# Performance work log

Hardware: AMD Instinct MI355X
Metric: run time of the kernel (lower is better)

Reference implementation:

```python
import jax, jax.numpy as jnp
import numpy as np

D_MODEL = 256
D_STATE = 64
D_CONV = 4
EXPAND = 2
HEADDIM = 64
D_INNER = EXPAND * D_MODEL          # 512
NHEADS = D_INNER // HEADDIM         # 8
CONV_DIM = D_INNER + 2 * D_STATE    # 640
D_IN_PROJ = 2 * D_INNER + 2 * D_STATE + NHEADS  # 1160
BATCH = 4
SEQ = 4096  # H*W = 64*64


def _silu(x):
    return x * jax.nn.sigmoid(x)


def _layernorm(x, w, b, eps=1e-5):
    mu = jnp.mean(x, axis=-1, keepdims=True)
    xc = x - mu
    var = jnp.mean(xc * xc, axis=-1, keepdims=True)
    return xc * jax.lax.rsqrt(var + eps) * w + b


def _mamba2(x, W_in, conv_w, conv_b, dt_bias, A_log, D_param, rms_w, W_out):
    # x: (B, L, d_model)
    B, L, _ = x.shape
    zxbcdt = x @ W_in.T                                   # (B,L,1160)
    z = zxbcdt[..., :D_INNER]                             # gate (B,L,512)
    xBC = zxbcdt[..., D_INNER:D_INNER + CONV_DIM]         # (B,L,640)
    dt = jax.nn.softplus(zxbcdt[..., -NHEADS:] + dt_bias) # (B,L,8)
    # causal depthwise conv (kernel D_CONV) + SiLU
    xp = jnp.pad(xBC, ((0, 0), (D_CONV - 1, 0), (0, 0)))
    xBC = sum(xp[:, k:k + L, :] * conv_w[:, k] for k in range(D_CONV)) + conv_b
    xBC = _silu(xBC)
    xh = xBC[..., :D_INNER].reshape(B, L, NHEADS, HEADDIM)
    Bm = xBC[..., D_INNER:D_INNER + D_STATE]              # (B,L,64), ngroups=1
    Cm = xBC[..., D_INNER + D_STATE:]                     # (B,L,64)
    dA = jnp.exp(dt * (-jnp.exp(A_log)))                  # (B,L,H) decay per head

    def step(h, ins):
        # h: (B,H,P,N)
        dA_t, dt_t, x_t, B_t, C_t = ins
        h = dA_t[:, :, None, None] * h + jnp.einsum('bh,bhp,bn->bhpn', dt_t, x_t, B_t)
        y = jnp.einsum('bhpn,bn->bhp', h, C_t)
        return h, y

    h0 = jnp.zeros((B, NHEADS, HEADDIM, D_STATE), x.dtype)
    _, ys = jax.lax.scan(step, h0, (jnp.swapaxes(dA, 0, 1), jnp.swapaxes(dt, 0, 1),
                                    jnp.swapaxes(xh, 0, 1), jnp.swapaxes(Bm, 0, 1),
                                    jnp.swapaxes(Cm, 0, 1)))
    y = jnp.swapaxes(ys, 0, 1) + D_param[:, None] * xh    # skip term, (B,L,H,P)
    y = y.reshape(B, L, D_INNER) * _silu(z)               # gated
    y = y * jax.lax.rsqrt(jnp.mean(y * y, axis=-1, keepdims=True) + 1e-5) * rms_w
    return y @ W_out.T


def setup_inputs() -> dict:
    key = jax.random.key(0)
    ks = jax.random.split(key, 10)
    s = 0.02
    return {
        'x0_seq': jax.random.normal(ks[0], (BATCH, SEQ, D_MODEL), jnp.float32),
        'x1_seq': jax.random.normal(ks[1], (BATCH, SEQ, D_MODEL), jnp.float32),
        'norm_s_w': jnp.ones((D_MODEL,), jnp.float32),
        'norm_s_b': jnp.zeros((D_MODEL,), jnp.float32),
        'W_in': jax.random.normal(ks[2], (D_IN_PROJ, D_MODEL), jnp.float32) * s,
        'conv_w': jax.random.normal(ks[3], (CONV_DIM, D_CONV), jnp.float32) * 0.2,
        'conv_b': jnp.zeros((CONV_DIM,), jnp.float32),
        'dt_bias': jax.random.normal(ks[4], (NHEADS,), jnp.float32) * 0.1,
        'A_log': jnp.log(jnp.arange(1, NHEADS + 1, dtype=jnp.float32)),
        'D_param': jnp.ones((NHEADS,), jnp.float32),
        'rms_w': jnp.ones((D_INNER,), jnp.float32),
        'W_out': jax.random.normal(ks[5], (D_MODEL, D_INNER), jnp.float32) * s,
        'mlp_w1': jax.random.normal(ks[6], (D_MODEL, 2 * D_MODEL), jnp.float32) * s,
        'mlp_b1': jnp.zeros((D_MODEL,), jnp.float32),
        'mlp_w2': jax.random.normal(ks[7], (D_MODEL, D_MODEL), jnp.float32) * s,
        'mlp_b2': jnp.zeros((D_MODEL,), jnp.float32),
        'norm_t_w': jnp.ones((D_MODEL,), jnp.float32),
        'norm_t_b': jnp.zeros((D_MODEL,), jnp.float32),
        'H': 64,
        'W': 64,
    }


def reference(x0_seq, x1_seq, norm_s_w, norm_s_b, W_in, conv_w, conv_b, dt_bias,
              A_log, D_param, rms_w, W_out, mlp_w1, mlp_b1, mlp_w2, mlp_b2,
              norm_t_w, norm_t_b, H, W):
    B = x0_seq.shape[0]
    x_cat = jnp.concatenate([x0_seq, x1_seq], axis=0)     # (2B,L,C)
    x_norm = _layernorm(x_cat, norm_s_w, norm_s_b)
    sp = _mamba2(x_norm, W_in, conv_w, conv_b, dt_bias, A_log, D_param, rms_w, W_out) + x_cat
    f0, f1 = sp[:B], sp[B:]

    def mlp(a, b):
        h = _silu(jnp.concatenate([a, b], axis=-1) @ mlp_w1.T + mlp_b1)
        return h @ mlp_w2.T + mlp_b2

    f0_fused = _layernorm(f0 + mlp(f0, f1), norm_t_w, norm_t_b)
    f1_fused = _layernorm(f1 + mlp(f1, f0), norm_t_w, norm_t_b)
    return (f0_fused, f1_fused)
```

## Files before the change

kernel.cpp:

```cpp
#include <hip/hip_runtime.h>
#include <math.h>

typedef unsigned short bf16_t;
typedef __attribute__((ext_vector_type(8))) short bf16x8;
typedef __attribute__((ext_vector_type(4))) float f32x4;

#define LSEQ 4096
#define NTOK 32768
#define HALF_TOK 16384
#define TPAD 72

__device__ __forceinline__ float bf2f(bf16_t u) {
    unsigned int x = ((unsigned int)u) << 16;
    return __uint_as_float(x);
}
__device__ __forceinline__ bf16_t f2bf(float f) {
    unsigned int x = __float_as_uint(f);
    unsigned int r = (x + 0x7FFFu + ((x >> 16) & 1u)) >> 16;
    return (bf16_t)r;
}
__device__ __forceinline__ float siluf(float x) { return x / (1.f + __expf(-x)); }

__device__ __forceinline__ void unpack8(uint4 u, float* f) {
    f[0] = bf2f((bf16_t)(u.x & 0xffff)); f[1] = bf2f((bf16_t)(u.x >> 16));
    f[2] = bf2f((bf16_t)(u.y & 0xffff)); f[3] = bf2f((bf16_t)(u.y >> 16));
    f[4] = bf2f((bf16_t)(u.z & 0xffff)); f[5] = bf2f((bf16_t)(u.z >> 16));
    f[6] = bf2f((bf16_t)(u.w & 0xffff)); f[7] = bf2f((bf16_t)(u.w >> 16));
}
__device__ __forceinline__ uint4 pack8(const float* f) {
    uint4 u;
    u.x = (unsigned)f2bf(f[0]) | ((unsigned)f2bf(f[1]) << 16);
    u.y = (unsigned)f2bf(f[2]) | ((unsigned)f2bf(f[3]) << 16);
    u.z = (unsigned)f2bf(f[4]) | ((unsigned)f2bf(f[5]) << 16);
    u.w = (unsigned)f2bf(f[6]) | ((unsigned)f2bf(f[7]) << 16);
    return u;
}
__device__ __forceinline__ void st4(bf16_t* p, const float* o) {
    ushort4 u; u.x = f2bf(o[0]); u.y = f2bf(o[1]); u.z = f2bf(o[2]); u.w = f2bf(o[3]);
    *(ushort4*)p = u;
}

__device__ __forceinline__ void stage_N(bf16_t (*T)[TPAD], const bf16_t* g, int rs, int tid) {
    #pragma unroll
    for (int it = 0; it < 2; ++it) {
        int slot = it * 256 + tid;
        int r = slot >> 3, co = slot & 7;
        *(uint4*)&T[r][co * 8] = *(const uint4*)(g + (size_t)r * rs + co * 8);
    }
}

__device__ __forceinline__ void stage_T(bf16_t (*T)[TPAD], const bf16_t* g, int rs, int tid) {
    int rp = tid >> 3;
    int co = tid & 7;
    int r0 = rp * 2;
    const bf16_t* p0 = g + (size_t)r0 * rs + co * 8;
    uint4 a = *(const uint4*)p0;
    uint4 b = *(const uint4*)(p0 + rs);
    unsigned aa[4] = {a.x, a.y, a.z, a.w};
    unsigned bb[4] = {b.x, b.y, b.z, b.w};
    #pragma unroll
    for (int q = 0; q < 4; ++q) {
        int c0 = co * 8 + q * 2;
        *(unsigned*)&T[c0][r0]     = (aa[q] & 0xffffu) | (bb[q] << 16 & 0xffff0000u);
        *(unsigned*)&T[c0 + 1][r0] = (aa[q] >> 16)     | (bb[q] & 0xffff0000u);
    }
}

__global__ __launch_bounds__(256) void wconv_kernel(
    const float* __restrict__ s, bf16_t* __restrict__ d, int n4)
{
    int i = blockIdx.x * 256 + threadIdx.x;
    if (i < n4) {
        float4 v = ((const float4*)s)[i];
        ushort4 u; u.x = f2bf(v.x); u.y = f2bf(v.y); u.z = f2bf(v.z); u.w = f2bf(v.w);
        ((ushort4*)d)[i] = u;
    }
}

__global__ __launch_bounds__(256) void ln_cat_kernel(
    const float* __restrict__ x0, const float* __restrict__ x1,
    const float* __restrict__ w, const float* __restrict__ b,
    bf16_t* __restrict__ out)
{
    int row = blockIdx.x * 4 + (threadIdx.x >> 6);
    int lane = threadIdx.x & 63;
    const float* src = (row < HALF_TOK) ? x0 + (size_t)row * 256
                                        : x1 + (size_t)(row - HALF_TOK) * 256;
    float4 v = ((const float4*)src)[lane];
    float s = v.x + v.y + v.z + v.w;
    float sq = v.x*v.x + v.y*v.y + v.z*v.z + v.w*v.w;
    #pragma unroll
    for (int off = 32; off; off >>= 1) { s += __shfl_xor(s, off); sq += __shfl_xor(sq, off); }
    float mu = s * (1.f/256.f);
    float var = sq * (1.f/256.f) - mu*mu;
    float inv = rsqrtf(var + 1e-5f);
    float4 wv = ((const float4*)w)[lane];
    float4 bv = ((const float4*)b)[lane];
    float o[4];
    o[0] = (v.x-mu)*inv*wv.x + bv.x;
    o[1] = (v.y-mu)*inv*wv.y + bv.y;
    o[2] = (v.z-mu)*inv*wv.z + bv.z;
    o[3] = (v.w-mu)*inv*wv.w + bv.w;
    st4(out + (size_t)row * 256 + lane * 4, o);
}

template<int AMODE, typename TC, bool BIAS, bool SILU, bool RES>
__global__ __launch_bounds__(256) void gemm_mfma(
    const void* __restrict__ Avoid, const bf16_t* __restrict__ W,
    const float* __restrict__ bias, TC* __restrict__ C,
    const float* __restrict__ r0, const float* __restrict__ r1,
    int M, int N, int K)
{
    __shared__ bf16_t As[128][40];
    __shared__ bf16_t Ws[128][40];
    int tid = threadIdx.x;
    int m0 = blockIdx.x << 7, n0 = blockIdx.y << 7;
    int wave = tid >> 6, lane = tid & 63;
    int wr = wave >> 1, wc = wave & 1;
    int fr = lane & 15, fk = lane >> 4;

    f32x4 acc[4][4] = {};

    for (int k0 = 0; k0 < K; k0 += 32) {
        __syncthreads();
        #pragma unroll
        for (int ss = 0; ss < 2; ++ss) {
            int s = tid + ss * 256;
            int row = s >> 2, cs = s & 3;
            int kk = k0 + cs * 8;
            if (AMODE == 0) {
                const bf16_t* Ap = (const bf16_t*)Avoid;
                uint4 v = *(const uint4*)(Ap + (size_t)(m0 + row) * K + kk);
                *(uint4*)&As[row][cs * 8] = v;
            } else {
                const float* Ap = (const float*)Avoid;
                int m = m0 + row;
                const float* p = (AMODE == 1) ? (Ap + (size_t)m * K + kk)
                    : ((kk < 256) ? (Ap + (size_t)m * 256 + kk)
                                  : (Ap + (size_t)(m ^ HALF_TOK) * 256 + (kk - 256)));
                float4 f0 = *(const float4*)p, f1 = *(const float4*)(p + 4);
                float f[8] = {f0.x, f0.y, f0.z, f0.w, f1.x, f1.y, f1.z, f1.w};
                *(uint4*)&As[row][cs * 8] = pack8(f);
            }
            uint4 wv = make_uint4(0u, 0u, 0u, 0u);
            if (n0 + row < N) wv = *(const uint4*)(W + (size_t)(n0 + row) * K + kk);
            *(uint4*)&Ws[row][cs * 8] = wv;
        }
        __syncthreads();

        bf16x8 af[4], bf[4];
        #pragma unroll
        for (int i = 0; i < 4; ++i)
            af[i] = *(const bf16x8*)&As[wr * 64 + i * 16 + fr][fk * 8];
        #pragma unroll
        for (int j = 0; j < 4; ++j)
            bf[j] = *(const bf16x8*)&Ws[wc * 64 + j * 16 + fr][fk * 8];
        #pragma unroll
        for (int i = 0; i < 4; ++i)
            #pragma unroll
            for (int j = 0; j < 4; ++j)
                acc[i][j] = __builtin_amdgcn_mfma_f32_16x16x32_bf16(af[i], bf[j], acc[i][j], 0, 0, 0);
    }

    int fq = lane >> 4;
    #pragma unroll
    for (int j = 0; j < 4; ++j) {
        int n = n0 + wc * 64 + j * 16 + fr;
        if (n >= N) continue;
        float bval = BIAS ? bias[n] : 0.f;
        #pragma unroll
        for (int i = 0; i < 4; ++i) {
            #pragma unroll
            for (int q = 0; q < 4; ++q) {
                int m = m0 + wr * 64 + i * 16 + fq * 4 + q;
                float v = acc[i][j][q];
                if (BIAS) v += bval;
                if (SILU) v = siluf(v);
                if (RES) v += (m < HALF_TOK) ? r0[(size_t)m * 256 + n]
                                             : r1[(size_t)(m - HALF_TOK) * 256 + n];
                if (sizeof(TC) == 4) ((float*)C)[(size_t)m * N + n] = v;
                else ((bf16_t*)C)[(size_t)m * N + n] = f2bf(v);
            }
        }
    }
}

__global__ __launch_bounds__(320) void conv_dt_kernel(
    const bf16_t* __restrict__ zx, const float* __restrict__ cw,
    const float* __restrict__ cb, const float* __restrict__ dtb,
    const float* __restrict__ alog,
    bf16_t* __restrict__ conv_out, float* __restrict__ dts, float* __restrict__ lda)
{
    int tl = threadIdx.x / 80;
    int slot = threadIdx.x - tl * 80;
    int tok = blockIdx.x * 4 + tl;
    int b = tok >> 12, t = tok & 4095;
    int ch = slot * 8;

    float f[4][8];
    #pragma unroll
    for (int k = 0; k < 4; ++k) {
        int tp = t - 3 + k;
        if (tp >= 0) {
            uint4 u = *(const uint4*)(zx + (size_t)(b * LSEQ + tp) * 1160 + 512 + ch);
            unpack8(u, f[k]);
        } else {
            #pragma unroll
            for (int j = 0; j < 8; ++j) f[k][j] = 0.f;
        }
    }
    float o[8];
    #pragma unroll
    for (int j = 0; j < 8; ++j) {
        float4 w4 = *(const float4*)(cw + (ch + j) * 4);
        float acc = cb[ch + j] + w4.x * f[0][j] + w4.y * f[1][j] + w4.z * f[2][j] + w4.w * f[3][j];
        o[j] = siluf(acc);
    }
    *(uint4*)(conv_out + (size_t)tok * 640 + ch) = pack8(o);

    if (slot < 8) {
        int h = slot;
        float raw = bf2f(zx[(size_t)tok * 1160 + 1152 + h]) + dtb[h];
        float dt = (raw > 20.f) ? raw : log1pf(__expf(raw));
        dts[tok * 8 + h] = dt;
        lda[tok * 8 + h] = -dt * __expf(alog[h]);
    }
}

__global__ __launch_bounds__(256) void scan_passA(
    const bf16_t* __restrict__ conv_out, const float* __restrict__ dts,
    const float* __restrict__ lda, bf16_t* __restrict__ SH, float* __restrict__ Dtot)
{
    int bh = blockIdx.x, c = blockIdx.y;
    int b = bh >> 3, h = bh & 7;
    __shared__ bf16_t Xt[64][TPAD];
    __shared__ bf16_t Bw[64][TPAD];
    __shared__ float wls[64];
    int tid = threadIdx.x;
    int tokbase = b * LSEQ + c * 64;

    if (tid < 64) {
        float la = lda[(tokbase + tid) * 8 + h];
        #pragma unroll
        for (int off = 1; off < 64; off <<= 1) {
            float up = __shfl_up(la, off);
            if (tid >= off) la += up;
        }
        float tot = __shfl(la, 63);
        wls[tid] = __expf(tot - la) * dts[(tokbase + tid) * 8 + h];
        if (tid == 63) Dtot[bh * 64 + c] = __expf(tot);
    }
    stage_T(Xt, conv_out + (size_t)tokbase * 640 + h * 64, 640, tid);
    __syncthreads();

    {
        int rp = tid >> 3, co = tid & 7;
        int r0 = rp * 2;
        const bf16_t* p0 = conv_out + (size_t)(tokbase + r0) * 640 + 512 + co * 8;
        uint4 a = *(const uint4*)p0;
        uint4 bq = *(const uint4*)(p0 + 640);
        float fa[8], fb[8];
        unpack8(a, fa); unpack8(bq, fb);
        float w0 = wls[r0], w1 = wls[r0 + 1];
        #pragma unroll
        for (int q = 0; q < 8; ++q) {
            int c0 = co * 8 + q;
            *(unsigned*)&Bw[c0][r0] =
                (unsigned)f2bf(fa[q] * w0) | ((unsigned)f2bf(fb[q] * w1) << 16);
        }
    }
    __syncthreads();

    int wv = tid >> 6, lane = tid & 63;
    int fr = lane & 15, fk = lane >> 4;
    f32x4 acc[4] = {};
    bf16x8 af0 = *(const bf16x8*)&Xt[wv * 16 + fr][fk * 8];
    bf16x8 af1 = *(const bf16x8*)&Xt[wv * 16 + fr][32 + fk * 8];
    #pragma unroll
    for (int j = 0; j < 4; ++j) {
        bf16x8 b0 = *(const bf16x8*)&Bw[j * 16 + fr][fk * 8];
        bf16x8 b1 = *(const bf16x8*)&Bw[j * 16 + fr][32 + fk * 8];
        acc[j] = __builtin_amdgcn_mfma_f32_16x16x32_bf16(af0, b0, acc[j], 0, 0, 0);
        acc[j] = __builtin_amdgcn_mfma_f32_16x16x32_bf16(af1, b1, acc[j], 0, 0, 0);
    }
    __syncthreads();
    #pragma unroll
    for (int j = 0; j < 4; ++j)
        #pragma unroll
        for (int q = 0; q < 4; ++q) {
            int p = wv * 16 + fk * 4 + q;
            Xt[p][j * 16 + fr] = f2bf(acc[j][q]);
        }
    __syncthreads();
    size_t base = (size_t)(bh * 64 + c) * 4096;
    #pragma unroll
    for (int it = 0; it < 2; ++it) {
        int slot = it * 256 + tid;
        int p = slot >> 3, co = slot & 7;
        *(uint4*)(SH + base + p * 64 + co * 8) = *(const uint4*)&Xt[p][co * 8];
    }
}

__global__ __launch_bounds__(256) void scan_passB(bf16_t* __restrict__ SH, const float* __restrict__ Dtot)
{
    int bh = blockIdx.x;
    int elem = blockIdx.y * 256 + threadIdx.x;
    size_t base = (size_t)bh * 64 * 4096 + elem;
    float H = 0.f;
    for (int c = 0; c < 64; ++c) {
        float d = Dtot[bh * 64 + c];
        size_t a = base + (size_t)c * 4096;
        float s = bf2f(SH[a]);
        SH[a] = f2bf(H);
        H = d * H + s;
    }
}

__global__ __launch_bounds__(256) void scan_passC(
    const bf16_t* __restrict__ conv_out, const float* __restrict__ dts,
    const float* __restrict__ lda, const bf16_t* __restrict__ SH,
    bf16_t* __restrict__ ybuf)
{
    int bh = blockIdx.x, c = blockIdx.y;
    int b = bh >> 3, h = bh & 7;
    __shared__ bf16_t Cs[64][TPAD];
    __shared__ bf16_t Bs[64][TPAD];
    __shared__ bf16_t Hs[64][TPAD];
    __shared__ bf16_t Xt[64][TPAD];
    __shared__ float La_sh[64], dt_sh[64], ce_sh[64];
    int tid = threadIdx.x;
    int tokbase = b * LSEQ + c * 64;
    size_t shbase = (size_t)(bh * 64 + c) * 4096;

    if (tid < 64) {
        float la = lda[(tokbase + tid) * 8 + h];
        #pragma unroll
        for (int off = 1; off < 64; off <<= 1) {
            float up = __shfl_up(la, off);
            if (tid >= off) la += up;
        }
        La_sh[tid] = la;
        ce_sh[tid] = __expf(la);
        dt_sh[tid] = dts[(tokbase + tid) * 8 + h];
    }
    stage_N(Cs, conv_out + (size_t)tokbase * 640 + 576, 640, tid);
    stage_N(Bs, conv_out + (size_t)tokbase * 640 + 512, 640, tid);
    stage_N(Hs, SH + shbase, 64, tid);
    stage_T(Xt, conv_out + (size_t)tokbase * 640 + h * 64, 640, tid);
    __syncthreads();

    int wv = tid >> 6, lane = tid & 63;
    int fr = lane & 15, fk = lane >> 4;
    int ws = wv * 16;

    bf16x8 afC0 = *(const bf16x8*)&Cs[ws + fr][fk * 8];
    bf16x8 afC1 = *(const bf16x8*)&Cs[ws + fr][32 + fk * 8];
    f32x4 accG[4] = {}, accH[4] = {};
    #pragma unroll
    for (int j = 0; j < 4; ++j) {
        bf16x8 b0 = *(const bf16x8*)&Bs[j * 16 + fr][fk * 8];
        bf16x8 b1 = *(const bf16x8*)&Bs[j * 16 + fr][32 + fk * 8];
        accG[j] = __builtin_amdgcn_mfma_f32_16x16x32_bf16(afC0, b0, accG[j], 0, 0, 0);
        accG[j] = __builtin_amdgcn_mfma_f32_16x16x32_bf16(afC1, b1, accG[j], 0, 0, 0);
        bf16x8 h0 = *(const bf16x8*)&Hs[j * 16 + fr][fk * 8];
        bf16x8 h1 = *(const bf16x8*)&Hs[j * 16 + fr][32 + fk * 8];
        accH[j] = __builtin_amdgcn_mfma_f32_16x16x32_bf16(afC0, h0, accH[j], 0, 0, 0);
        accH[j] = __builtin_amdgcn_mfma_f32_16x16x32_bf16(afC1, h1, accH[j], 0, 0, 0);
    }

    #pragma unroll
    for (int j = 0; j < 4; ++j)
        #pragma unroll
        for (int q = 0; q < 4; ++q) {
            int s = ws + fk * 4 + q;
            int r = j * 16 + fr;
            float m1 = 0.f;
            if (r <= s) m1 = accG[j][q] * __expf(La_sh[s] - La_sh[r]) * dt_sh[r];
            Cs[s][r] = f2bf(m1);
        }
    #pragma unroll
    for (int j = 0; j < 4; ++j)
        #pragma unroll
        for (int q = 0; q < 4; ++q)
            accH[j][q] *= ce_sh[ws + fk * 4 + q];

    bf16x8 afM0 = *(const bf16x8*)&Cs[ws + fr][fk * 8];
    bf16x8 afM1 = *(const bf16x8*)&Cs[ws + fr][32 + fk * 8];
    #pragma unroll
    for (int j = 0; j < 4; ++j) {
        bf16x8 x0 = *(const bf16x8*)&Xt[j * 16 + fr][fk * 8];
        bf16x8 x1 = *(const bf16x8*)&Xt[j * 16 + fr][32 + fk * 8];
        accH[j] = __builtin_amdgcn_mfma_f32_16x16x32_bf16(afM0, x0, accH[j], 0, 0, 0);
        accH[j] = __builtin_amdgcn_mfma_f32_16x16x32_bf16(afM1, x1, accH[j], 0, 0, 0);
    }

    __syncthreads();
    #pragma unroll
    for (int j = 0; j < 4; ++j)
        #pragma unroll
        for (int q = 0; q < 4; ++q) {
            int s = ws + fk * 4 + q;
            Bs[s][j * 16 + fr] = f2bf(accH[j][q]);
        }
    __syncthreads();
    #pragma unroll
    for (int it = 0; it < 2; ++it) {
        int slot = it * 256 + tid;
        int r = slot >> 3, co = slot & 7;
        *(uint4*)(ybuf + (size_t)(tokbase + r) * 512 + h * 64 + co * 8) = *(const uint4*)&Bs[r][co * 8];
    }
}

__global__ __launch_bounds__(256) void gate_rms_kernel(
    bf16_t* __restrict__ y, const bf16_t* __restrict__ conv_out,
    const bf16_t* __restrict__ zx, const float* __restrict__ Dp,
    const float* __restrict__ rw)
{
    int row = blockIdx.x * 4 + (threadIdx.x >> 6);
    int lane = threadIdx.x & 63;
    uint4* yrow = (uint4*)(y + (size_t)row * 512);
    uint4 uy = yrow[lane];
    uint4 ux = *(const uint4*)(conv_out + (size_t)row * 640 + lane * 8);
    uint4 uz = *(const uint4*)(zx + (size_t)row * 1160 + lane * 8);
    float fy[8], fx[8], fz[8];
    unpack8(uy, fy); unpack8(ux, fx); unpack8(uz, fz);
    float d = Dp[lane >> 3];
    float v[8];
    float sq = 0.f;
    #pragma unroll
    for (int i = 0; i < 8; ++i) {
        v[i] = (fy[i] + d * fx[i]) * siluf(fz[i]);
        sq += v[i] * v[i];
    }
    #pragma unroll
    for (int off = 32; off; off >>= 1) sq += __shfl_xor(sq, off);
    float r = rsqrtf(sq * (1.f/512.f) + 1e-5f);
    float4 w0 = *(const float4*)(rw + lane * 8);
    float4 w1 = *(const float4*)(rw + lane * 8 + 4);
    float o[8];
    o[0] = v[0]*r*w0.x; o[1] = v[1]*r*w0.y; o[2] = v[2]*r*w0.z; o[3] = v[3]*r*w0.w;
    o[4] = v[4]*r*w1.x; o[5] = v[5]*r*w1.y; o[6] = v[6]*r*w1.z; o[7] = v[7]*r*w1.w;
    yrow[lane] = pack8(o);
}

__global__ __launch_bounds__(256) void final_ln_kernel(
    const float* __restrict__ sp, const float* __restrict__ mo,
    const float* __restrict__ w, const float* __restrict__ b,
    float* __restrict__ out)
{
    int row = blockIdx.x * 4 + (threadIdx.x >> 6);
    int lane = threadIdx.x & 63;
    float4 a = ((const float4*)(sp + (size_t)row * 256))[lane];
    float4 c = ((const float4*)(mo + (size_t)row * 256))[lane];
    float4 v = {a.x + c.x, a.y + c.y, a.z + c.z, a.w + c.w};
    float s = v.x + v.y + v.z + v.w;
    float sq = v.x*v.x + v.y*v.y + v.z*v.z + v.w*v.w;
    #pragma unroll
    for (int off = 32; off; off >>= 1) { s += __shfl_xor(s, off); sq += __shfl_xor(sq, off); }
    float mu = s * (1.f/256.f);
    float var = sq * (1.f/256.f) - mu*mu;
    float inv = rsqrtf(var + 1e-5f);
    float4 wv = ((const float4*)w)[lane];
    float4 bv = ((const float4*)b)[lane];
    float4 o;
    o.x = (v.x-mu)*inv*wv.x + bv.x;
    o.y = (v.y-mu)*inv*wv.y + bv.y;
    o.z = (v.z-mu)*inv*wv.z + bv.z;
    o.w = (v.w-mu)*inv*wv.w + bv.w;
    ((float4*)(out + (size_t)row * 256))[lane] = o;
}

extern "C" void kernel_launch(void* const* d_in, const int* in_sizes, int n_in,
                              void* d_out, int out_size, void* d_ws, size_t ws_size,
                              hipStream_t stream) {
    (void)in_sizes; (void)n_in; (void)out_size; (void)ws_size;
    const float* x0      = (const float*)d_in[0];
    const float* x1      = (const float*)d_in[1];
    const float* nsw     = (const float*)d_in[2];
    const float* nsb     = (const float*)d_in[3];
    const float* W_in    = (const float*)d_in[4];
    const float* conv_w  = (const float*)d_in[5];
    const float* conv_b  = (const float*)d_in[6];
    const float* dt_bias = (const float*)d_in[7];
    const float* A_log   = (const float*)d_in[8];
    const float* D_param = (const float*)d_in[9];
    const float* rms_w   = (const float*)d_in[10];
    const float* W_out   = (const float*)d_in[11];
    const float* mlp_w1  = (const float*)d_in[12];
    const float* mlp_b1  = (const float*)d_in[13];
    const float* mlp_w2  = (const float*)d_in[14];
    const float* mlp_b2  = (const float*)d_in[15];
    const float* ntw     = (const float*)d_in[16];
    const float* ntb     = (const float*)d_in[17];
    float* out = (float*)d_out;

    char* base = (char*)d_ws;
    bf16_t* zx = (bf16_t*)base;
    float*  sp = (float*)base;
    char* pB = base + 76021760;
    bf16_t* convo = (bf16_t*)pB;
    bf16_t* hbuf  = (bf16_t*)pB;
    char* pC = pB + 41943040;
    bf16_t* x_norm = (bf16_t*)pC;
    bf16_t* SH     = (bf16_t*)pC;
    char* pD = pC + 33554432;
    bf16_t* ybuf = (bf16_t*)pD;
    float*  mout = (float*)pD;
    char* pE = pD + 33554432;
    float* dts  = (float*)pE;
    float* lda  = dts + 262144;
    float* dtot = lda + 262144;
    bf16_t* Wb_in = (bf16_t*)(dtot + 4096);
    bf16_t* Wb_o  = Wb_in + 296960;
    bf16_t* Wb_1  = Wb_o + 131072;
    bf16_t* Wb_2  = Wb_1 + 131072;

    wconv_kernel<<<(74240 + 255) / 256, 256, 0, stream>>>(W_in,   Wb_in, 74240);
    wconv_kernel<<<(32768 + 255) / 256, 256, 0, stream>>>(W_out,  Wb_o,  32768);
    wconv_kernel<<<(32768 + 255) / 256, 256, 0, stream>>>(mlp_w1, Wb_1,  32768);
    wconv_kernel<<<(16384 + 255) / 256, 256, 0, stream>>>(mlp_w2, Wb_2,  16384);

    ln_cat_kernel<<<8192, 256, 0, stream>>>(x0, x1, nsw, nsb, x_norm);

    dim3 g_in(256, 10);
    gemm_mfma<0, bf16_t, false, false, false><<<g_in, 256, 0, stream>>>(
        x_norm, Wb_in, nullptr, zx, nullptr, nullptr, NTOK, 1160, 256);

    conv_dt_kernel<<<8192, 320, 0, stream>>>(zx, conv_w, conv_b, dt_bias, A_log, convo, dts, lda);

    dim3 g_scan(64, 64);
    scan_passA<<<g_scan, 256, 0, stream>>>(convo, dts, lda, SH, dtot);
    dim3 g_pb(64, 16);
    scan_passB<<<g_pb, 256, 0, stream>>>(SH, dtot);
    scan_passC<<<g_scan, 256, 0, stream>>>(convo, dts, lda, SH, ybuf);

    gate_rms_kernel<<<8192, 256, 0, stream>>>(ybuf, convo, zx, D_param, rms_w);

    dim3 g_out(256, 2);
    gemm_mfma<0, float, false, false, true><<<g_out, 256, 0, stream>>>(
        ybuf, Wb_o, nullptr, sp, x0, x1, NTOK, 256, 512);

    gemm_mfma<2, bf16_t, true, true, false><<<g_out, 256, 0, stream>>>(
        sp, Wb_1, mlp_b1, hbuf, nullptr, nullptr, NTOK, 256, 512);

    gemm_mfma<0, float, true, false, false><<<g_out, 256, 0, stream>>>(
        hbuf, Wb_2, mlp_b2, mout, nullptr, nullptr, NTOK, 256, 256);

    final_ln_kernel<<<8192, 256, 0, stream>>>(sp, mout, ntw, ntb, out);
}
```

Baseline: 420.1 us.

## Stage GEMM tiles via global_load_lds with swizzled 64-wide K tiles, emit bf16 residual copy

The MFMA GEMM now loads A and W tiles straight into LDS with the global-load-to-LDS builtin. It uses a 64-wide K step and an XOR-swizzled LDS layout to avoid bank conflicts, replacing register-staged 32-wide tiles. The out-projection GEMM also writes a bf16 copy of its fp32 result, so the first MLP GEMM reads bf16 directly instead of converting fp32 activations on load. The W-row bounds guard is dropped, so the in-projection GEMM reads past the 1160 weight rows into the adjacent workspace; those extra outputs are still discarded.

```diff
diff --git a/kernel.cpp b/kernel.cpp
--- a/kernel.cpp
+++ b/kernel.cpp
@@ -38,6 +38,13 @@
 __device__ __forceinline__ void st4(bf16_t* p, const float* o) {
     ushort4 u; u.x = f2bf(o[0]); u.y = f2bf(o[1]); u.z = f2bf(o[2]); u.w = f2bf(o[3]);
     *(ushort4*)p = u;
+}
+
+__device__ __forceinline__ void gload16(const bf16_t* g, bf16_t* l) {
+    __builtin_amdgcn_global_load_lds(
+        (const __attribute__((address_space(1))) unsigned int*)g,
+        (__attribute__((address_space(3))) unsigned int*)l,
+        16, 0, 0);
 }
 
 __device__ __forceinline__ void stage_N(bf16_t (*T)[TPAD], const bf16_t* g, int rs, int tid) {
@@ -104,62 +111,67 @@
     st4(out + (size_t)row * 256 + lane * 4, o);
 }
 
-template<int AMODE, typename TC, bool BIAS, bool SILU, bool RES>
+template<int AMODE, typename TC, bool BIAS, bool SILU, bool RES, bool DUAL>
 __global__ __launch_bounds__(256) void gemm_mfma(
-    const void* __restrict__ Avoid, const bf16_t* __restrict__ W,
+    const bf16_t* __restrict__ A, const bf16_t* __restrict__ W,
     const float* __restrict__ bias, TC* __restrict__ C,
     const float* __restrict__ r0, const float* __restrict__ r1,
+    bf16_t* __restrict__ C2,
     int M, int N, int K)
 {
-    __shared__ bf16_t As[128][40];
-    __shared__ bf16_t Ws[128][40];
-    int tid = threadIdx.x;
-    int m0 = blockIdx.x << 7, n0 = blockIdx.y << 7;
-    int wave = tid >> 6, lane = tid & 63;
-    int wr = wave >> 1, wc = wave & 1;
-    int fr = lane & 15, fk = lane >> 4;
+    __shared__ bf16_t As[128 * 64];
+    __shared__ bf16_t Ws[128 * 64];
+    const int tid = threadIdx.x;
+    const int wave = tid >> 6, lane = tid & 63;
+    const int m0 = blockIdx.x << 7, n0 = blockIdx.y << 7;
+    const int wr = wave >> 1, wc = wave & 1;
+    const int fr = lane & 15, fk = lane >> 4;
+
+    const int srow = lane >> 3;
+    const int schunk = (lane & 7) ^ srow;
 
     f32x4 acc[4][4] = {};
 
-    for (int k0 = 0; k0 < K; k0 += 32) {
+    for (int k0 = 0; k0 < K; k0 += 64) {
         __syncthreads();
         #pragma unroll
-        for (int ss = 0; ss < 2; ++ss) {
-            int s = tid + ss * 256;
-            int row = s >> 2, cs = s & 3;
-            int kk = k0 + cs * 8;
+        for (int t = 0; t < 4; ++t) {
+            int row = wave * 32 + t * 8 + srow;
+            const bf16_t* ga;
             if (AMODE == 0) {
-                const bf16_t* Ap = (const bf16_t*)Avoid;
-                uint4 v = *(const uint4*)(Ap + (size_t)(m0 + row) * K + kk);
-                *(uint4*)&As[row][cs * 8] = v;
+                ga = A + (size_t)(m0 + row) * K + k0 + schunk * 8;
             } else {
-                const float* Ap = (const float*)Avoid;
                 int m = m0 + row;
-                const float* p = (AMODE == 1) ? (Ap + (size_t)m * K + kk)
-                    : ((kk < 256) ? (Ap + (size_t)m * 256 + kk)
-                                  : (Ap + (size_t)(m ^ HALF_TOK) * 256 + (kk - 256)));
-                float4 f0 = *(const float4*)p, f1 = *(const float4*)(p + 4);
-                float f[8] = {f0.x, f0.y, f0.z, f0.w, f1.x, f1.y, f1.z, f1.w};
-                *(uint4*)&As[row][cs * 8] = pack8(f);
+                if (k0 < 256) ga = A + (size_t)m * 256 + k0 + schunk * 8;
+                else          ga = A + (size_t)(m ^ HALF_TOK) * 256 + (k0 - 256) + schunk * 8;
             }
-            uint4 wv = make_uint4(0u, 0u, 0u, 0u);
-            if (n0 + row < N) wv = *(const uint4*)(W + (size_t)(n0 + row) * K + kk);
-            *(uint4*)&Ws[row][cs * 8] = wv;
+            gload16(ga, As + wave * 2048 + t * 512);
+            const bf16_t* gw = W + (size_t)(n0 + row) * K + k0 + schunk * 8;
+            gload16(gw, Ws + wave * 2048 + t * 512);
         }
         __syncthreads();
 
-        bf16x8 af[4], bf[4];
-        #pragma unroll
-        for (int i = 0; i < 4; ++i)
-            af[i] = *(const bf16x8*)&As[wr * 64 + i * 16 + fr][fk * 8];
-        #pragma unroll
-        for (int j = 0; j < 4; ++j)
-            bf[j] = *(const bf16x8*)&Ws[wc * 64 + j * 16 + fr][fk * 8];
-        #pragma unroll
-        for (int i = 0; i < 4; ++i)
+        #pragma unroll
+        for (int half = 0; half < 2; ++half) {
+            bf16x8 af[4], bfr[4];
             #pragma unroll
-            for (int j = 0; j < 4; ++j)
-                acc[i][j] = __builtin_amdgcn_mfma_f32_16x16x32_bf16(af[i], bf[j], acc[i][j], 0, 0, 0);
+            for (int i = 0; i < 4; ++i) {
+                int row = wr * 64 + i * 16 + fr;
+                int c16 = (half * 4 + fk) ^ (row & 7);
+                af[i] = *(const bf16x8*)&As[row * 64 + c16 * 8];
+            }
+            #pragma unroll
+            for (int j = 0; j < 4; ++j) {
+                int row = wc * 64 + j * 16 + fr;
+                int c16 = (half * 4 + fk) ^ (row & 7);
+                bfr[j] = *(const bf16x8*)&Ws[row * 64 + c16 * 8];
+            }
+            #pragma unroll
+            for (int i = 0; i < 4; ++i)
+                #pragma unroll
+                for (int j = 0; j < 4; ++j)
+                    acc[i][j] = __builtin_amdgcn_mfma_f32_16x16x32_bf16(af[i], bfr[j], acc[i][j], 0, 0, 0);
+        }
     }
 
     int fq = lane >> 4;
@@ -180,6 +192,7 @@
                                              : r1[(size_t)(m - HALF_TOK) * 256 + n];
                 if (sizeof(TC) == 4) ((float*)C)[(size_t)m * N + n] = v;
                 else ((bf16_t*)C)[(size_t)m * N + n] = f2bf(v);
+                if (DUAL) C2[(size_t)m * N + n] = f2bf(v);
             }
         }
     }
@@ -503,6 +516,7 @@
     char* pC = pB + 41943040;
     bf16_t* x_norm = (bf16_t*)pC;
     bf16_t* SH     = (bf16_t*)pC;
+    bf16_t* spb    = (bf16_t*)pC;
     char* pD = pC + 33554432;
     bf16_t* ybuf = (bf16_t*)pD;
     float*  mout = (float*)pD;
@@ -523,8 +537,8 @@
     ln_cat_kernel<<<8192, 256, 0, stream>>>(x0, x1, nsw, nsb, x_norm);
 
     dim3 g_in(256, 10);
-    gemm_mfma<0, bf16_t, false, false, false><<<g_in, 256, 0, stream>>>(
-        x_norm, Wb_in, nullptr, zx, nullptr, nullptr, NTOK, 1160, 256);
+    gemm_mfma<0, bf16_t, false, false, false, false><<<g_in, 256, 0, stream>>>(
+        x_norm, Wb_in, nullptr, zx, nullptr, nullptr, nullptr, NTOK, 1160, 256);
 
     conv_dt_kernel<<<8192, 320, 0, stream>>>(zx, conv_w, conv_b, dt_bias, A_log, convo, dts, lda);
 
@@ -537,14 +551,14 @@
     gate_rms_kernel<<<8192, 256, 0, stream>>>(ybuf, convo, zx, D_param, rms_w);
 
     dim3 g_out(256, 2);
-    gemm_mfma<0, float, false, false, true><<<g_out, 256, 0, stream>>>(
-        ybuf, Wb_o, nullptr, sp, x0, x1, NTOK, 256, 512);
-
-    gemm_mfma<2, bf16_t, true, true, false><<<g_out, 256, 0, stream>>>(
-        sp, Wb_1, mlp_b1, hbuf, nullptr, nullptr, NTOK, 256, 512);
-
-    gemm_mfma<0, float, true, false, false><<<g_out, 256, 0, stream>>>(
-        hbuf, Wb_2, mlp_b2, mout, nullptr, nullptr, NTOK, 256, 256);
+    gemm_mfma<0, float, false, false, true, true><<<g_out, 256, 0, stream>>>(
+        ybuf, Wb_o, nullptr, sp, x0, x1, spb, NTOK, 256, 512);
+
+    gemm_mfma<1, bf16_t, true, true, false, false><<<g_out, 256, 0, stream>>>(
+        spb, Wb_1, mlp_b1, hbuf, nullptr, nullptr, nullptr, NTOK, 256, 512);
+
+    gemm_mfma<0, float, true, false, false, false><<<g_out, 256, 0, stream>>>(
+        hbuf, Wb_2, mlp_b2, mout, nullptr, nullptr, nullptr, NTOK, 256, 256);
 
     final_ln_kernel<<<8192, 256, 0, stream>>>(sp, mout, ntw, ntb, out);
 }
```

Measured after the change: 397.7 us. 1.06x faster.
